# Optimization experiments

Hardware: AMD Instinct MI355X
Metric: run time of the kernel (lower is better)

Reference implementation:

```python
import jax, jax.numpy as jnp
import numpy as np

DIM = 1024
NUM_HEADS = 8
HEAD_DIM = 64
QK_DIM = NUM_HEADS * HEAD_DIM  # 512
B, S = 4, 1024


def setup_inputs() -> dict:
    key = jax.random.key(0)
    k1, k2, k3, k4, k5 = jax.random.split(key, 5)
    x = jax.random.normal(k1, (B, S, DIM), dtype=jnp.float32)
    mask = jax.random.randint(k2, (B, S), 0, 2).astype(bool)
    rotator = jax.random.normal(k3, (B, S, HEAD_DIM, HEAD_DIM), dtype=jnp.float32)
    # Linear weights stored as [in, out] for x @ W
    w_t = jax.random.normal(k4, (DIM, 2 * QK_DIM + DIM), dtype=jnp.float32) * (DIM ** -0.5)
    w_o = jax.random.normal(k5, (DIM, DIM), dtype=jnp.float32) * (DIM ** -0.5)
    return {"x": x, "mask": mask, "rotator": rotator, "w_t": w_t, "w_o": w_o}


def taylor_atn_fn(qs, ks, vs, mask):
    # 2nd-order Taylor approximation of softmax attention:
    # exp(s) ~= 1 + s + s^2/2, with invalid keys masked out.
    scale = HEAD_DIM ** -0.5
    s = jnp.einsum('bqhd,bkhd->bhqk', qs, ks) * scale  # [B,H,S,S]
    scores = 1.0 + s + 0.5 * s * s
    scores = scores * mask[:, None, None, :].astype(scores.dtype)  # mask keys
    denom = jnp.maximum(jnp.sum(scores, axis=-1), 1e-6)            # [B,H,Q]
    out = jnp.einsum('bhqk,bkhd->bqhd', scores, vs)
    out = out / jnp.transpose(denom, (0, 2, 1))[..., None]         # [B,Q,H,vd]
    return out.reshape(out.shape[0], out.shape[1], -1)


def reference(x, mask, rotator, w_t, w_o):
    t = x @ w_t                                   # [B,S,2*QK+DIM]
    Bx, Sx = t.shape[0], t.shape[1]
    qs = t[..., :QK_DIM].reshape(Bx, Sx, NUM_HEADS, HEAD_DIM)
    ks = t[..., QK_DIM:2 * QK_DIM].reshape(Bx, Sx, NUM_HEADS, HEAD_DIM)
    vs = t[..., 2 * QK_DIM:].reshape(Bx, Sx, NUM_HEADS, -1)
    m = mask[..., None, None]
    # masked per-position rotation: q -> R q, k -> R^T k
    qs = jnp.where(m, jnp.einsum('bsij,bshj->bshi', rotator, qs), qs)
    ks = jnp.where(m, jnp.einsum('bsij,bshi->bshj', rotator, ks), ks)
    out = taylor_atn_fn(qs, ks, vs, mask)
    return out @ w_o
```

## Files before the change

### kernel.cpp

```cpp
#include <hip/hip_runtime.h>
#include <cstdint>
#include <cstddef>

#define DIMX  1024
#define NH    8
#define HD    64
#define QKD   512
#define VDD   128
#define BATCH 4
#define SEQ   1024
#define NPOS  (BATCH*SEQ)
#define TW    (2*QKD + DIMX)
#define SCALE 0.125f

typedef __bf16 bf16x8 __attribute__((ext_vector_type(8)));
typedef float  f32x4  __attribute__((ext_vector_type(4)));
typedef float  f32x16 __attribute__((ext_vector_type(16)));

__device__ __forceinline__ ushort f2bf(float f) {
    unsigned b = __float_as_uint(f);
    return (ushort)((b + 0x7FFFu + ((b >> 16) & 1u)) >> 16);
}
__device__ __forceinline__ float bf2f(ushort u) {
    return __uint_as_float((unsigned)u << 16);
}

__device__ __forceinline__ unsigned cvtpk(float lo, float hi) {
    unsigned r;
    asm("v_cvt_pk_bf16_f32 %0, %1, %2" : "=v"(r) : "v"(lo), "v"(hi));
    return r;
}

__device__ __forceinline__ void plswap(unsigned &a, unsigned &b) {
    asm("v_permlane32_swap_b32 %0, %1" : "+v"(a), "+v"(b));
}

#define GLD16(src, dst) __builtin_amdgcn_global_load_lds(                      \
    (const __attribute__((address_space(1))) unsigned int*)(src),              \
    (__attribute__((address_space(3))) unsigned int*)(dst), 16, 0, 0)

#define SW(row, col) ((row)*64 + ((col) ^ (((row)&7)<<3)))

__device__ __forceinline__ int2 xcd_swz(int gx, int gy) {
    const int nwg = gx * gy;
    int id = blockIdx.y * gx + blockIdx.x;
    id = (id & 7) * (nwg >> 3) + (id >> 3);
    return make_int2(id % gx, id / gx);
}

__global__ __launch_bounds__(256)
void cast_bf16(const float* __restrict__ in, ushort* __restrict__ out, int n4)
{
    const int i = blockIdx.x * 256 + threadIdx.x;
    if (i >= n4) return;
    float4 v = *(const float4*)(in + (size_t)i * 4);
    ushort4 o;
    o.x = f2bf(v.x); o.y = f2bf(v.y); o.z = f2bf(v.z); o.w = f2bf(v.w);
    *(ushort4*)(out + (size_t)i * 4) = o;
}

__global__ __launch_bounds__(256)
void transpose_cast(const float* __restrict__ W, ushort* __restrict__ WT,
                    int K, int N)
{
    __shared__ float tile[32][33];
    const int bn = blockIdx.x * 32;
    const int bk = blockIdx.y * 32;
    const int tx = threadIdx.x & 31;
    const int ty = threadIdx.x >> 5;
    #pragma unroll
    for (int i = ty; i < 32; i += 8)
        tile[i][tx] = W[(size_t)(bk + i) * N + bn + tx];
    __syncthreads();
    #pragma unroll
    for (int i = ty; i < 32; i += 8)
        WT[(size_t)(bn + i) * K + bk + tx] = f2bf(tile[tx][i]);
}

__global__ __launch_bounds__(256, 2)
void gemm_qkv(const ushort* __restrict__ A, const ushort* __restrict__ BT,
              ushort* __restrict__ t1b, ushort* __restrict__ Vt)
{
    const int K = DIMX, N = TW;
    __shared__ __align__(16) ushort lA[128 * 32];
    __shared__ __align__(16) ushort lB[128 * 32];

    const int2 bij = xcd_swz(N/128, NPOS/128);
    const int tid  = threadIdx.x;
    const int lane = tid & 63;
    const int wave = tid >> 6;
    const int wr   = wave >> 1;
    const int wc   = wave & 1;
    const int bm   = bij.y * 128;
    const int bn   = bij.x * 128;

    const int r0 = wave * 32 + (lane >> 2);
    const int kc = (lane & 3) * 8;
    const ushort* a0 = A  + (size_t)(bm + r0) * K + kc;
    const ushort* a1 = A  + (size_t)(bm + r0 + 16) * K + kc;
    const ushort* b0 = BT + (size_t)(bn + r0) * K + kc;
    const ushort* b1 = BT + (size_t)(bn + r0 + 16) * K + kc;
    ushort* lA0 = lA + wave * 1024;
    ushort* lA1 = lA0 + 512;
    ushort* lB0 = lB + wave * 1024;
    ushort* lB1 = lB0 + 512;

    const int fr = lane & 15;
    const int kh = (lane >> 4) * 8;
    const ushort* ra = lA + (wr * 64 + fr) * 32 + kh;
    const ushort* rb = lB + (wc * 64 + fr) * 32 + kh;

    f32x4 acc[4][4] = {};

    for (int k0 = 0; k0 < K; k0 += 32) {
        GLD16(a0 + k0, lA0);
        GLD16(a1 + k0, lA1);
        GLD16(b0 + k0, lB0);
        GLD16(b1 + k0, lB1);
        asm volatile("s_waitcnt vmcnt(0)" ::: "memory");
        __syncthreads();
        bf16x8 af[4], bfr[4];
        #pragma unroll
        for (int m = 0; m < 4; ++m) af[m]  = *(const bf16x8*)(ra + m * 512);
        #pragma unroll
        for (int n = 0; n < 4; ++n) bfr[n] = *(const bf16x8*)(rb + n * 512);
        #pragma unroll
        for (int m = 0; m < 4; ++m)
            #pragma unroll
            for (int n = 0; n < 4; ++n)
                acc[m][n] = __builtin_amdgcn_mfma_f32_16x16x32_bf16(
                    af[m], bfr[n], acc[m][n], 0, 0, 0);
        __syncthreads();
    }

    const int orow = (lane >> 4) * 4;
    if (bn < 1024) {
        #pragma unroll
        for (int m = 0; m < 4; ++m)
            #pragma unroll
            for (int n = 0; n < 4; ++n) {
                ushort* dst = t1b + (size_t)(bm + wr * 64 + m * 16 + orow) * 1024
                                  + bn + wc * 64 + n * 16 + fr;
                #pragma unroll
                for (int q = 0; q < 4; ++q)
                    dst[(size_t)q * 1024] = f2bf(acc[m][n][q]);
            }
    } else {
        #pragma unroll
        for (int m = 0; m < 4; ++m)
            #pragma unroll
            for (int n = 0; n < 4; ++n) {
                const int row0 = bm + wr * 64 + m * 16 + orow;
                const int cv   = bn + wc * 64 + n * 16 + fr - 1024;
                const int hh = cv >> 7, vd = cv & 127;
                const int bb = row0 >> 10, ss = row0 & 1023;
                ushort o4[4];
                #pragma unroll
                for (int q = 0; q < 4; ++q) o4[q] = f2bf(acc[m][n][q]);
                *(ushort4*)&Vt[((size_t)(bb*NH + hh)*VDD + vd)*SEQ + ss] =
                    *(ushort4*)o4;
            }
    }
}

__global__ __launch_bounds__(256, 2)
void gemm_bf16_mfma(const ushort* __restrict__ A, const ushort* __restrict__ BT,
                    float* __restrict__ C, int M, int N, int K)
{
    __shared__ __align__(16) ushort lA[128 * 32];
    __shared__ __align__(16) ushort lB[128 * 32];

    const int2 bij = xcd_swz(N/128, M/128);
    const int tid  = threadIdx.x;
    const int lane = tid & 63;
    const int wave = tid >> 6;
    const int wr   = wave >> 1;
    const int wc   = wave & 1;
    const int bm   = bij.y * 128;
    const int bn   = bij.x * 128;

    const int r0 = wave * 32 + (lane >> 2);
    const int kc = (lane & 3) * 8;
    const ushort* a0 = A  + (size_t)(bm + r0) * K + kc;
    const ushort* a1 = A  + (size_t)(bm + r0 + 16) * K + kc;
    const ushort* b0 = BT + (size_t)(bn + r0) * K + kc;
    const ushort* b1 = BT + (size_t)(bn + r0 + 16) * K + kc;
    ushort* lA0 = lA + wave * 1024;
    ushort* lA1 = lA0 + 512;
    ushort* lB0 = lB + wave * 1024;
    ushort* lB1 = lB0 + 512;

    const int fr = lane & 15;
    const int kh = (lane >> 4) * 8;
    const ushort* ra = lA + (wr * 64 + fr) * 32 + kh;
    const ushort* rb = lB + (wc * 64 + fr) * 32 + kh;

    f32x4 acc[4][4] = {};

    for (int k0 = 0; k0 < K; k0 += 32) {
        GLD16(a0 + k0, lA0);
        GLD16(a1 + k0, lA1);
        GLD16(b0 + k0, lB0);
        GLD16(b1 + k0, lB1);
        asm volatile("s_waitcnt vmcnt(0)" ::: "memory");
        __syncthreads();
        bf16x8 af[4], bfr[4];
        #pragma unroll
        for (int m = 0; m < 4; ++m) af[m]  = *(const bf16x8*)(ra + m * 512);
        #pragma unroll
        for (int n = 0; n < 4; ++n) bfr[n] = *(const bf16x8*)(rb + n * 512);
        #pragma unroll
        for (int m = 0; m < 4; ++m)
            #pragma unroll
            for (int n = 0; n < 4; ++n)
                acc[m][n] = __builtin_amdgcn_mfma_f32_16x16x32_bf16(
                    af[m], bfr[n], acc[m][n], 0, 0, 0);
        __syncthreads();
    }

    const int orow = (lane >> 4) * 4;
    #pragma unroll
    for (int m = 0; m < 4; ++m)
        #pragma unroll
        for (int n = 0; n < 4; ++n) {
            float* dst = C + (size_t)(bm + wr * 64 + m * 16 + orow) * N
                           + bn + wc * 64 + n * 16 + fr;
            #pragma unroll
            for (int q = 0; q < 4; ++q)
                dst[(size_t)q * N] = acc[m][n][q];
        }
}

__global__ __launch_bounds__(256)
void rotate_pack_qk(const ushort* __restrict__ t1b, const int* __restrict__ mask,
                    const float* __restrict__ rot, ushort* __restrict__ Qb,
                    ushort* __restrict__ Kb)
{
    const int p   = blockIdx.x;
    const int tid = threadIdx.x;
    const int b = p >> 10, s = p & 1023;
    const bool rotated = (mask[p] != 0);

    __shared__ float R[64][69];
    __shared__ float qv[QKD];
    __shared__ float kv[QKD];

    const ushort* tq = t1b + (size_t)p * 1024;
    {
        ushort2 q2 = *(const ushort2*)(tq + tid*2);
        ushort2 k2 = *(const ushort2*)(tq + QKD + tid*2);
        qv[tid*2]   = bf2f(q2.x); qv[tid*2+1] = bf2f(q2.y);
        kv[tid*2]   = bf2f(k2.x); kv[tid*2+1] = bf2f(k2.y);
        if (rotated) {
            const float* Rg = rot + (size_t)p * 4096;
            const int base = tid * 16;
            const int r = base >> 6, c = base & 63;
            #pragma unroll
            for (int x = 0; x < 16; x += 4) {
                float4 v = *(const float4*)(Rg + base + x);
                R[r][c+x+0] = v.x; R[r][c+x+1] = v.y;
                R[r][c+x+2] = v.z; R[r][c+x+3] = v.w;
            }
        }
    }
    __syncthreads();

    #pragma unroll
    for (int ph = 0; ph < 2; ++ph) {
        const int h = (tid >> 6) + ph*4;
        const int i = tid & 63;
        const float* qh  = &qv[h*64];
        const float* kh2 = &kv[h*64];
        float aq, ak;
        if (rotated) {
            aq = 0.f; ak = 0.f;
            #pragma unroll 8
            for (int j = 0; j < 64; ++j) {
                aq = fmaf(R[i][j], qh[j], aq);
                ak = fmaf(R[j][i], kh2[j], ak);
            }
        } else {
            aq = qh[i]; ak = kh2[i];
        }
        const size_t dst = ((size_t)(b*NH + h)*SEQ + s)*HD + i;
        Qb[dst] = f2bf(aq * SCALE);
        Kb[dst] = f2bf(ak);
    }
}

__global__ __launch_bounds__(256, 2)
void taylor_attn_mfma(const ushort* __restrict__ Qb, const ushort* __restrict__ Kb,
                      const ushort* __restrict__ Vt, const int* __restrict__ mask,
                      ushort* __restrict__ attn)
{
    const int bh  = blockIdx.x;
    const int qt  = blockIdx.y;
    const int b   = bh >> 3, h = bh & 7;
    const int tid = threadIdx.x;
    const int lane = tid & 63;
    const int wave = tid >> 6;
    const int kh  = wave >> 1;
    const int qg  = wave & 1;
    const int l31 = lane & 31;
    const int g   = lane >> 5;

    __shared__ __align__(16) ushort smem[32768];
    __shared__ float mskAll[SEQ];
    __shared__ float dpart[64];
    __shared__ float dinv2[64];

    ushort* Ksp = smem + kh * 8192;
    ushort* Vsp = smem + 16384 + kh * 8192;
    float*  comb = (float*)smem;

    {
        int4 mv = *(const int4*)(mask + b*SEQ + tid*4);
        float4 f = make_float4(mv.x ? 1.f : 0.f, mv.y ? 1.f : 0.f,
                               mv.z ? 1.f : 0.f, mv.w ? 1.f : 0.f);
        *(float4*)&mskAll[tid*4] = f;
    }

    const ushort* qrow = Qb + ((size_t)bh*SEQ + qt*64 + qg*32 + l31) * HD + g*8;
    bf16x8 qf[4];
    #pragma unroll
    for (int ds = 0; ds < 4; ++ds) qf[ds] = *(const bf16x8*)(qrow + ds*16);

    const int sub  = lane >> 3;
    const int scol = ((lane & 7) * 8) ^ (sub << 3);
    const ushort* Kbase = Kb + (size_t)bh*SEQ*HD;
    const ushort* Vbase = Vt + (size_t)bh*VDD*SEQ;

#define ISSUE_K(buf, ktn) do {                                                 \
    _Pragma("unroll")                                                          \
    for (int i_ = 0; i_ < 4; ++i_)                                             \
        GLD16(Kbase + ((size_t)(ktn)*64 + 8*(qg*4+i_) + sub)*HD + scol,        \
              Ksp + (buf)*4096 + (qg*4+i_)*512);                               \
} while (0)
#define ISSUE_V(ktn) do {                                                      \
    _Pragma("unroll")                                                          \
    for (int i_ = 0; i_ < 8; ++i_)                                             \
        GLD16(Vbase + (size_t)(8*(qg*8+i_) + sub)*SEQ + (ktn)*64 + scol,       \
              Vsp + (qg*8+i_)*512);                                            \
} while (0)

    f32x16 acc[4] = {};
    float dacc = 0.f;

    __syncthreads();
    ISSUE_K(0, kh*8);

    for (int it = 0; it < 8; ++it) {
        const int kt = kh*8 + it;
        const int cb = it & 1;
        ISSUE_V(kt);
        if (it < 7) {
            ISSUE_K(cb ^ 1, kt + 1);
            asm volatile("s_waitcnt vmcnt(12)" ::: "memory");
        } else {
            asm volatile("s_waitcnt vmcnt(8)"  ::: "memory");
        }
        __builtin_amdgcn_s_barrier();

        f32x16 sf0 = {}, sf1 = {};
        __builtin_amdgcn_s_setprio(1);
        #pragma unroll
        for (int ds = 0; ds < 4; ++ds) {
            const int dc = ds*16 + g*8;
            bf16x8 kf0 = *(const bf16x8*)&Ksp[cb*4096 + SW(l31, dc)];
            bf16x8 kf1 = *(const bf16x8*)&Ksp[cb*4096 + SW(32 + l31, dc)];
            sf0 = __builtin_amdgcn_mfma_f32_32x32x16_bf16(kf0, qf[ds], sf0, 0, 0, 0);
            sf1 = __builtin_amdgcn_mfma_f32_32x32x16_bf16(kf1, qf[ds], sf1, 0, 0, 0);
        }
        __builtin_amdgcn_s_setprio(0);

        const float* mrow = mskAll + kt*64;
        unsigned w0[8], w1[8];
        float dadd = 0.f;
        #pragma unroll
        for (int rr = 0; rr < 4; ++rr) {
            const float4 mqa = *(const float4*)&mrow[8*rr + 4*g];
            const float4 mqb = *(const float4*)&mrow[32 + 8*rr + 4*g];
            float s0 = sf0[rr*4+0], s1 = sf0[rr*4+1];
            float s2 = sf0[rr*4+2], s3 = sf0[rr*4+3];
            float c0 = fmaf(fmaf(0.5f*s0, s0, s0), mqa.x, mqa.x);
            float c1 = fmaf(fmaf(0.5f*s1, s1, s1), mqa.y, mqa.y);
            float c2 = fmaf(fmaf(0.5f*s2, s2, s2), mqa.z, mqa.z);
            float c3 = fmaf(fmaf(0.5f*s3, s3, s3), mqa.w, mqa.w);
            float t0 = sf1[rr*4+0], t1 = sf1[rr*4+1];
            float t2 = sf1[rr*4+2], t3 = sf1[rr*4+3];
            float d0 = fmaf(fmaf(0.5f*t0, t0, t0), mqb.x, mqb.x);
            float d1 = fmaf(fmaf(0.5f*t1, t1, t1), mqb.y, mqb.y);
            float d2 = fmaf(fmaf(0.5f*t2, t2, t2), mqb.z, mqb.z);
            float d3 = fmaf(fmaf(0.5f*t3, t3, t3), mqb.w, mqb.w);
            dadd += ((c0+c1)+(c2+c3)) + ((d0+d1)+(d2+d3));
            w0[rr*2+0] = cvtpk(c0, c1);
            w0[rr*2+1] = cvtpk(c2, c3);
            w1[rr*2+0] = cvtpk(d0, d1);
            w1[rr*2+1] = cvtpk(d2, d3);
        }
        dacc += dadd;
        plswap(w0[0], w0[2]); plswap(w0[1], w0[3]);
        plswap(w0[4], w0[6]); plswap(w0[5], w0[7]);
        plswap(w1[0], w1[2]); plswap(w1[1], w1[3]);
        plswap(w1[4], w1[6]); plswap(w1[5], w1[7]);

        if (it < 7) asm volatile("s_waitcnt vmcnt(4)" ::: "memory");
        else        asm volatile("s_waitcnt vmcnt(0)" ::: "memory");
        __builtin_amdgcn_s_barrier();

        __builtin_amdgcn_s_setprio(1);
        #pragma unroll
        for (int kq = 0; kq < 4; ++kq) {
            union { unsigned u[4]; bf16x8 v; } pu;
            if (kq == 0)      { pu.u[0]=w0[0]; pu.u[1]=w0[1]; pu.u[2]=w0[2]; pu.u[3]=w0[3]; }
            else if (kq == 1) { pu.u[0]=w0[4]; pu.u[1]=w0[5]; pu.u[2]=w0[6]; pu.u[3]=w0[7]; }
            else if (kq == 2) { pu.u[0]=w1[0]; pu.u[1]=w1[1]; pu.u[2]=w1[2]; pu.u[3]=w1[3]; }
            else              { pu.u[0]=w1[4]; pu.u[1]=w1[5]; pu.u[2]=w1[6]; pu.u[3]=w1[7]; }
            const int kcol = kq*16 + g*8;
            acc[0] = __builtin_amdgcn_mfma_f32_32x32x16_bf16(
                pu.v, *(const bf16x8*)&Vsp[SW(      l31, kcol)], acc[0], 0, 0, 0);
            acc[1] = __builtin_amdgcn_mfma_f32_32x32x16_bf16(
                pu.v, *(const bf16x8*)&Vsp[SW( 32 + l31, kcol)], acc[1], 0, 0, 0);
            acc[2] = __builtin_amdgcn_mfma_f32_32x32x16_bf16(
                pu.v, *(const bf16x8*)&Vsp[SW( 64 + l31, kcol)], acc[2], 0, 0, 0);
            acc[3] = __builtin_amdgcn_mfma_f32_32x32x16_bf16(
                pu.v, *(const bf16x8*)&Vsp[SW( 96 + l31, kcol)], acc[3], 0, 0, 0);
        }
        __builtin_amdgcn_s_setprio(0);
        __builtin_amdgcn_s_barrier();
    }
#undef ISSUE_K
#undef ISSUE_V

    const float dhalf = dacc + __shfl_xor(dacc, 32);

    if (kh == 1) {
        float* cbp = comb + qg * 4096;
        #pragma unroll
        for (int vb = 0; vb < 4; ++vb)
            #pragma unroll
            for (int rr = 0; rr < 4; ++rr) {
                float4 v = make_float4(acc[vb][rr*4+0], acc[vb][rr*4+1],
                                       acc[vb][rr*4+2], acc[vb][rr*4+3]);
                *(float4*)&cbp[(vb*32 + l31)*32 + 4*g + 8*rr] = v;
            }
        if (lane < 32) dpart[qg*32 + l31] = dhalf;
    }
    __syncthreads();
    if (kh == 0) {
        float* cbp = comb + qg * 4096;
        const float dtot = dhalf + dpart[qg*32 + l31];
        if (lane < 32) dinv2[qg*32 + l31] = 1.f / fmaxf(dtot, 1e-6f);
        #pragma unroll
        for (int vb = 0; vb < 4; ++vb)
            #pragma unroll
            for (int rr = 0; rr < 4; ++rr) {
                float4 v = *(const float4*)&cbp[(vb*32 + l31)*32 + 4*g + 8*rr];
                acc[vb][rr*4+0] += v.x; acc[vb][rr*4+1] += v.y;
                acc[vb][rr*4+2] += v.z; acc[vb][rr*4+3] += v.w;
            }
        float inv[16];
        #pragma unroll
        for (int rr = 0; rr < 4; ++rr) {
            float4 iv = *(const float4*)&dinv2[qg*32 + 8*rr + 4*g];
            inv[rr*4+0] = iv.x; inv[rr*4+1] = iv.y;
            inv[rr*4+2] = iv.z; inv[rr*4+3] = iv.w;
        }
        ushort* obase = attn + ((size_t)(b*SEQ + qt*64 + qg*32)) * DIMX
                      + h*VDD + l31;
        #pragma unroll
        for (int vb = 0; vb < 4; ++vb)
            #pragma unroll
            for (int rr = 0; rr < 4; ++rr)
                #pragma unroll
                for (int j = 0; j < 4; ++j) {
                    const int q = 4*g + 8*rr + j;
                    obase[(size_t)q*DIMX + vb*32] = f2bf(acc[vb][rr*4+j] * inv[rr*4+j]);
                }
    }
}

extern "C" void kernel_launch(void* const* d_in, const int* in_sizes, int n_in,
                              void* d_out, int out_size, void* d_ws, size_t ws_size,
                              hipStream_t stream)
{
    const float* x    = (const float*)d_in[0];
    const int*   mask = (const int*)d_in[1];
    const float* rot  = (const float*)d_in[2];
    const float* w_t  = (const float*)d_in[3];
    const float* w_o  = (const float*)d_in[4];
    float* out = (float*)d_out;

    ushort* t1b    = (ushort*)d_ws;
    ushort* xbf    = t1b + (size_t)NPOS * 1024;
    ushort* attnbf = xbf;
    ushort* wtT    = xbf + (size_t)NPOS * DIMX;
    ushort* woT    = wtT + (size_t)TW * DIMX;
    ushort* Qb     = woT + (size_t)DIMX * DIMX;
    ushort* Kb     = Qb  + (size_t)BATCH * NH * SEQ * HD;
    ushort* Vtp    = Kb  + (size_t)BATCH * NH * SEQ * HD;

    cast_bf16<<<(NPOS*DIMX/4 + 255)/256, 256, 0, stream>>>(x, xbf, NPOS*DIMX/4);
    transpose_cast<<<dim3(TW/32, DIMX/32),   256, 0, stream>>>(w_t, wtT, DIMX, TW);
    transpose_cast<<<dim3(DIMX/32, DIMX/32), 256, 0, stream>>>(w_o, woT, DIMX, DIMX);

    gemm_qkv<<<dim3(TW/128, NPOS/128), 256, 0, stream>>>(xbf, wtT, t1b, Vtp);
    rotate_pack_qk<<<NPOS, 256, 0, stream>>>(t1b, mask, rot, Qb, Kb);
    taylor_attn_mfma<<<dim3(BATCH*NH, SEQ/64), 256, 0, stream>>>(Qb, Kb, Vtp, mask, attnbf);
    gemm_bf16_mfma<<<dim3(DIMX/128, NPOS/128), 256, 0, stream>>>(attnbf, woT, out, NPOS, DIMX, DIMX);
}
```

Measured before the change: 111.4 us.

## Restructure Taylor attention to 2 waves each owning full key range

The attention kernel drops from 4 waves (split across two key halves plus two query groups) to 2 waves, each handling 32 queries over all 1024 keys in 32-key tiles with its own private K/V LDS buffers. This removes the cross-wave block barriers inside the loop and the final LDS reduction of partial accumulators and denominators. V tiles use a new 32-column swizzle. In exchange, each workgroup has half as many waves, the per-wave loop is longer, and the serialized waitcnt pattern per iteration may expose more memory latency.

After: 120.6 us. 1.08x slower.

```diff
diff --git a/kernel.cpp b/kernel.cpp
--- a/kernel.cpp
+++ b/kernel.cpp
@@ -40,6 +40,7 @@
     (__attribute__((address_space(3))) unsigned int*)(dst), 16, 0, 0)
 
 #define SW(row, col) ((row)*64 + ((col) ^ (((row)&7)<<3)))
+#define SW32(row, col) ((row)*32 + ((col) ^ ((((row)>>1)&3)<<3)))
 
 __device__ __forceinline__ int2 xcd_swz(int gx, int gy) {
     const int nwg = gx * gy;
@@ -288,7 +289,7 @@
     }
 }
 
-__global__ __launch_bounds__(256, 2)
+__global__ __launch_bounds__(128, 2)
 void taylor_attn_mfma(const ushort* __restrict__ Qb, const ushort* __restrict__ Kb,
                       const ushort* __restrict__ Vt, const int* __restrict__ mask,
                       ushort* __restrict__ attn)
@@ -299,185 +300,141 @@
     const int tid = threadIdx.x;
     const int lane = tid & 63;
     const int wave = tid >> 6;
-    const int kh  = wave >> 1;
-    const int qg  = wave & 1;
     const int l31 = lane & 31;
     const int g   = lane >> 5;
 
-    __shared__ __align__(16) ushort smem[32768];
+    __shared__ __align__(16) ushort smem[16384];
     __shared__ float mskAll[SEQ];
-    __shared__ float dpart[64];
-    __shared__ float dinv2[64];
-
-    ushort* Ksp = smem + kh * 8192;
-    ushort* Vsp = smem + 16384 + kh * 8192;
-    float*  comb = (float*)smem;
+    __shared__ float dinvw[2][32];
+
+    ushort* Ksp = smem + wave * 4096;
+    ushort* Vsp = smem + 8192 + wave * 4096;
 
     {
-        int4 mv = *(const int4*)(mask + b*SEQ + tid*4);
-        float4 f = make_float4(mv.x ? 1.f : 0.f, mv.y ? 1.f : 0.f,
-                               mv.z ? 1.f : 0.f, mv.w ? 1.f : 0.f);
-        *(float4*)&mskAll[tid*4] = f;
-    }
-
-    const ushort* qrow = Qb + ((size_t)bh*SEQ + qt*64 + qg*32 + l31) * HD + g*8;
+        int4 m0 = *(const int4*)(mask + b*SEQ + tid*8);
+        int4 m1 = *(const int4*)(mask + b*SEQ + tid*8 + 4);
+        float4 f0 = make_float4(m0.x ? 1.f : 0.f, m0.y ? 1.f : 0.f,
+                                m0.z ? 1.f : 0.f, m0.w ? 1.f : 0.f);
+        float4 f1 = make_float4(m1.x ? 1.f : 0.f, m1.y ? 1.f : 0.f,
+                                m1.z ? 1.f : 0.f, m1.w ? 1.f : 0.f);
+        *(float4*)&mskAll[tid*8]     = f0;
+        *(float4*)&mskAll[tid*8 + 4] = f1;
+    }
+
+    const ushort* qrow = Qb + ((size_t)bh*SEQ + qt*64 + wave*32 + l31) * HD + g*8;
     bf16x8 qf[4];
     #pragma unroll
     for (int ds = 0; ds < 4; ++ds) qf[ds] = *(const bf16x8*)(qrow + ds*16);
 
-    const int sub  = lane >> 3;
-    const int scol = ((lane & 7) * 8) ^ (sub << 3);
+    const int ksub  = lane >> 3;
+    const int kcolS = ((lane & 7) * 8) ^ (ksub << 3);
+    const int vrow  = lane >> 2;
+    const int vcolS = ((lane & 3) * 8) ^ (((lane >> 3) & 3) << 3);
     const ushort* Kbase = Kb + (size_t)bh*SEQ*HD;
     const ushort* Vbase = Vt + (size_t)bh*VDD*SEQ;
 
 #define ISSUE_K(buf, ktn) do {                                                 \
     _Pragma("unroll")                                                          \
     for (int i_ = 0; i_ < 4; ++i_)                                             \
-        GLD16(Kbase + ((size_t)(ktn)*64 + 8*(qg*4+i_) + sub)*HD + scol,        \
-              Ksp + (buf)*4096 + (qg*4+i_)*512);                               \
+        GLD16(Kbase + ((size_t)(ktn)*32 + 8*i_ + ksub)*HD + kcolS,             \
+              Ksp + (buf)*2048 + i_*512);                                      \
 } while (0)
 #define ISSUE_V(ktn) do {                                                      \
     _Pragma("unroll")                                                          \
     for (int i_ = 0; i_ < 8; ++i_)                                             \
-        GLD16(Vbase + (size_t)(8*(qg*8+i_) + sub)*SEQ + (ktn)*64 + scol,       \
-              Vsp + (qg*8+i_)*512);                                            \
+        GLD16(Vbase + (size_t)(16*i_ + vrow)*SEQ + (ktn)*32 + vcolS,           \
+              Vsp + i_*512);                                                   \
 } while (0)
 
     f32x16 acc[4] = {};
     float dacc = 0.f;
 
     __syncthreads();
-    ISSUE_K(0, kh*8);
-
-    for (int it = 0; it < 8; ++it) {
-        const int kt = kh*8 + it;
-        const int cb = it & 1;
+    ISSUE_K(0, 0);
+    asm volatile("s_waitcnt vmcnt(0)" ::: "memory");
+
+    #pragma unroll 2
+    for (int kt = 0; kt < 32; ++kt) {
+        const int cb = kt & 1;
+        asm volatile("s_waitcnt lgkmcnt(0)" ::: "memory");
         ISSUE_V(kt);
-        if (it < 7) {
-            ISSUE_K(cb ^ 1, kt + 1);
-            asm volatile("s_waitcnt vmcnt(12)" ::: "memory");
-        } else {
-            asm volatile("s_waitcnt vmcnt(8)"  ::: "memory");
-        }
-        __builtin_amdgcn_s_barrier();
-
-        f32x16 sf0 = {}, sf1 = {};
+        if (kt < 31) ISSUE_K(cb ^ 1, kt + 1);
+
+        f32x16 sf0 = {};
         __builtin_amdgcn_s_setprio(1);
         #pragma unroll
         for (int ds = 0; ds < 4; ++ds) {
-            const int dc = ds*16 + g*8;
-            bf16x8 kf0 = *(const bf16x8*)&Ksp[cb*4096 + SW(l31, dc)];
-            bf16x8 kf1 = *(const bf16x8*)&Ksp[cb*4096 + SW(32 + l31, dc)];
-            sf0 = __builtin_amdgcn_mfma_f32_32x32x16_bf16(kf0, qf[ds], sf0, 0, 0, 0);
-            sf1 = __builtin_amdgcn_mfma_f32_32x32x16_bf16(kf1, qf[ds], sf1, 0, 0, 0);
+            bf16x8 kf = *(const bf16x8*)&Ksp[cb*2048 + SW(l31, ds*16 + g*8)];
+            sf0 = __builtin_amdgcn_mfma_f32_32x32x16_bf16(kf, qf[ds], sf0, 0, 0, 0);
         }
         __builtin_amdgcn_s_setprio(0);
 
-        const float* mrow = mskAll + kt*64;
-        unsigned w0[8], w1[8];
+        const float* mrow = mskAll + kt*32;
+        unsigned w[8];
         float dadd = 0.f;
         #pragma unroll
         for (int rr = 0; rr < 4; ++rr) {
-            const float4 mqa = *(const float4*)&mrow[8*rr + 4*g];
-            const float4 mqb = *(const float4*)&mrow[32 + 8*rr + 4*g];
+            const float4 mq = *(const float4*)&mrow[8*rr + 4*g];
             float s0 = sf0[rr*4+0], s1 = sf0[rr*4+1];
             float s2 = sf0[rr*4+2], s3 = sf0[rr*4+3];
-            float c0 = fmaf(fmaf(0.5f*s0, s0, s0), mqa.x, mqa.x);
-            float c1 = fmaf(fmaf(0.5f*s1, s1, s1), mqa.y, mqa.y);
-            float c2 = fmaf(fmaf(0.5f*s2, s2, s2), mqa.z, mqa.z);
-            float c3 = fmaf(fmaf(0.5f*s3, s3, s3), mqa.w, mqa.w);
-            float t0 = sf1[rr*4+0], t1 = sf1[rr*4+1];
-            float t2 = sf1[rr*4+2], t3 = sf1[rr*4+3];
-            float d0 = fmaf(fmaf(0.5f*t0, t0, t0), mqb.x, mqb.x);
-            float d1 = fmaf(fmaf(0.5f*t1, t1, t1), mqb.y, mqb.y);
-            float d2 = fmaf(fmaf(0.5f*t2, t2, t2), mqb.z, mqb.z);
-            float d3 = fmaf(fmaf(0.5f*t3, t3, t3), mqb.w, mqb.w);
-            dadd += ((c0+c1)+(c2+c3)) + ((d0+d1)+(d2+d3));
-            w0[rr*2+0] = cvtpk(c0, c1);
-            w0[rr*2+1] = cvtpk(c2, c3);
-            w1[rr*2+0] = cvtpk(d0, d1);
-            w1[rr*2+1] = cvtpk(d2, d3);
+            float c0 = fmaf(fmaf(0.5f*s0, s0, s0), mq.x, mq.x);
+            float c1 = fmaf(fmaf(0.5f*s1, s1, s1), mq.y, mq.y);
+            float c2 = fmaf(fmaf(0.5f*s2, s2, s2), mq.z, mq.z);
+            float c3 = fmaf(fmaf(0.5f*s3, s3, s3), mq.w, mq.w);
+            dadd += (c0 + c1) + (c2 + c3);
+            w[rr*2+0] = cvtpk(c0, c1);
+            w[rr*2+1] = cvtpk(c2, c3);
         }
         dacc += dadd;
-        plswap(w0[0], w0[2]); plswap(w0[1], w0[3]);
-        plswap(w0[4], w0[6]); plswap(w0[5], w0[7]);
-        plswap(w1[0], w1[2]); plswap(w1[1], w1[3]);
-        plswap(w1[4], w1[6]); plswap(w1[5], w1[7]);
-
-        if (it < 7) asm volatile("s_waitcnt vmcnt(4)" ::: "memory");
-        else        asm volatile("s_waitcnt vmcnt(0)" ::: "memory");
-        __builtin_amdgcn_s_barrier();
+        plswap(w[0], w[2]); plswap(w[1], w[3]);
+        plswap(w[4], w[6]); plswap(w[5], w[7]);
+
+        if (kt < 31) asm volatile("s_waitcnt vmcnt(4)" ::: "memory");
+        else         asm volatile("s_waitcnt vmcnt(0)" ::: "memory");
 
         __builtin_amdgcn_s_setprio(1);
         #pragma unroll
-        for (int kq = 0; kq < 4; ++kq) {
+        for (int kq = 0; kq < 2; ++kq) {
             union { unsigned u[4]; bf16x8 v; } pu;
-            if (kq == 0)      { pu.u[0]=w0[0]; pu.u[1]=w0[1]; pu.u[2]=w0[2]; pu.u[3]=w0[3]; }
-            else if (kq == 1) { pu.u[0]=w0[4]; pu.u[1]=w0[5]; pu.u[2]=w0[6]; pu.u[3]=w0[7]; }
-            else if (kq == 2) { pu.u[0]=w1[0]; pu.u[1]=w1[1]; pu.u[2]=w1[2]; pu.u[3]=w1[3]; }
-            else              { pu.u[0]=w1[4]; pu.u[1]=w1[5]; pu.u[2]=w1[6]; pu.u[3]=w1[7]; }
+            if (kq == 0) { pu.u[0]=w[0]; pu.u[1]=w[1]; pu.u[2]=w[2]; pu.u[3]=w[3]; }
+            else         { pu.u[0]=w[4]; pu.u[1]=w[5]; pu.u[2]=w[6]; pu.u[3]=w[7]; }
             const int kcol = kq*16 + g*8;
             acc[0] = __builtin_amdgcn_mfma_f32_32x32x16_bf16(
-                pu.v, *(const bf16x8*)&Vsp[SW(      l31, kcol)], acc[0], 0, 0, 0);
+                pu.v, *(const bf16x8*)&Vsp[SW32(      l31, kcol)], acc[0], 0, 0, 0);
             acc[1] = __builtin_amdgcn_mfma_f32_32x32x16_bf16(
-                pu.v, *(const bf16x8*)&Vsp[SW( 32 + l31, kcol)], acc[1], 0, 0, 0);
+                pu.v, *(const bf16x8*)&Vsp[SW32( 32 + l31, kcol)], acc[1], 0, 0, 0);
             acc[2] = __builtin_amdgcn_mfma_f32_32x32x16_bf16(
-                pu.v, *(const bf16x8*)&Vsp[SW( 64 + l31, kcol)], acc[2], 0, 0, 0);
+                pu.v, *(const bf16x8*)&Vsp[SW32( 64 + l31, kcol)], acc[2], 0, 0, 0);
             acc[3] = __builtin_amdgcn_mfma_f32_32x32x16_bf16(
-                pu.v, *(const bf16x8*)&Vsp[SW( 96 + l31, kcol)], acc[3], 0, 0, 0);
+                pu.v, *(const bf16x8*)&Vsp[SW32( 96 + l31, kcol)], acc[3], 0, 0, 0);
         }
         __builtin_amdgcn_s_setprio(0);
-        __builtin_amdgcn_s_barrier();
+        if (kt < 31) asm volatile("s_waitcnt vmcnt(0)" ::: "memory");
     }
 #undef ISSUE_K
 #undef ISSUE_V
 
-    const float dhalf = dacc + __shfl_xor(dacc, 32);
-
-    if (kh == 1) {
-        float* cbp = comb + qg * 4096;
-        #pragma unroll
-        for (int vb = 0; vb < 4; ++vb)
-            #pragma unroll
-            for (int rr = 0; rr < 4; ++rr) {
-                float4 v = make_float4(acc[vb][rr*4+0], acc[vb][rr*4+1],
-                                       acc[vb][rr*4+2], acc[vb][rr*4+3]);
-                *(float4*)&cbp[(vb*32 + l31)*32 + 4*g + 8*rr] = v;
+    const float dfull = dacc + __shfl_xor(dacc, 32);
+    if (lane < 32) dinvw[wave][l31] = 1.f / fmaxf(dfull, 1e-6f);
+    float inv[16];
+    #pragma unroll
+    for (int rr = 0; rr < 4; ++rr) {
+        float4 iv = *(const float4*)&dinvw[wave][8*rr + 4*g];
+        inv[rr*4+0] = iv.x; inv[rr*4+1] = iv.y;
+        inv[rr*4+2] = iv.z; inv[rr*4+3] = iv.w;
+    }
+
+    ushort* obase = attn + ((size_t)(b*SEQ + qt*64 + wave*32)) * DIMX
+                  + h*VDD + l31;
+    #pragma unroll
+    for (int vb = 0; vb < 4; ++vb)
+        #pragma unroll
+        for (int rr = 0; rr < 4; ++rr)
+            #pragma unroll
+            for (int j = 0; j < 4; ++j) {
+                const int q = 4*g + 8*rr + j;
+                obase[(size_t)q*DIMX + vb*32] = f2bf(acc[vb][rr*4+j] * inv[rr*4+j]);
             }
-        if (lane < 32) dpart[qg*32 + l31] = dhalf;
-    }
-    __syncthreads();
-    if (kh == 0) {
-        float* cbp = comb + qg * 4096;
-        const float dtot = dhalf + dpart[qg*32 + l31];
-        if (lane < 32) dinv2[qg*32 + l31] = 1.f / fmaxf(dtot, 1e-6f);
-        #pragma unroll
-        for (int vb = 0; vb < 4; ++vb)
-            #pragma unroll
-            for (int rr = 0; rr < 4; ++rr) {
-                float4 v = *(const float4*)&cbp[(vb*32 + l31)*32 + 4*g + 8*rr];
-                acc[vb][rr*4+0] += v.x; acc[vb][rr*4+1] += v.y;
-                acc[vb][rr*4+2] += v.z; acc[vb][rr*4+3] += v.w;
-            }
-        float inv[16];
-        #pragma unroll
-        for (int rr = 0; rr < 4; ++rr) {
-            float4 iv = *(const float4*)&dinv2[qg*32 + 8*rr + 4*g];
-            inv[rr*4+0] = iv.x; inv[rr*4+1] = iv.y;
-            inv[rr*4+2] = iv.z; inv[rr*4+3] = iv.w;
-        }
-        ushort* obase = attn + ((size_t)(b*SEQ + qt*64 + qg*32)) * DIMX
-                      + h*VDD + l31;
-        #pragma unroll
-        for (int vb = 0; vb < 4; ++vb)
-            #pragma unroll
-            for (int rr = 0; rr < 4; ++rr)
-                #pragma unroll
-                for (int j = 0; j < 4; ++j) {
-                    const int q = 4*g + 8*rr + j;
-                    obase[(size_t)q*DIMX + vb*32] = f2bf(acc[vb][rr*4+j] * inv[rr*4+j]);
-                }
-    }
 }
 
 extern "C" void kernel_launch(void* const* d_in, const int* in_sizes, int n_in,
@@ -506,6 +463,6 @@
 
     gemm_qkv<<<dim3(TW/128, NPOS/128), 256, 0, stream>>>(xbf, wtT, t1b, Vtp);
     rotate_pack_qk<<<NPOS, 256, 0, stream>>>(t1b, mask, rot, Qb, Kb);
-    taylor_attn_mfma<<<dim3(BATCH*NH, SEQ/64), 256, 0, stream>>>(Qb, Kb, Vtp, mask, attnbf);
+    taylor_attn_mfma<<<dim3(BATCH*NH, SEQ/64), 128, 0, stream>>>(Qb, Kb, Vtp, mask, attnbf);
     gemm_bf16_mfma<<<dim3(DIMX/128, NPOS/128), 256, 0, stream>>>(attnbf, woT, out, NPOS, DIMX, DIMX);
 }
```

## Merge prep kernels and widen GEMM K-tile to 64 with swizzled LDS

Applied to the files above, without the earlier changes.

Replaces the three preprocessing launches (x cast and two weight transposes) with one prep_all kernel that dispatches on block index, which removes two launches. Both GEMMs now stage 64-wide K tiles with XOR-swizzled LDS addressing instead of 32-wide. This halves the barrier and wait iterations and is meant to reduce LDS bank conflicts on fragment reads. Shared memory per block doubles to 32KB, which could limit occupancy.

Result: faster. 98.34 us (-11.7%).

```diff
diff --git a/kernel.cpp b/kernel.cpp
--- a/kernel.cpp
+++ b/kernel.cpp
@@ -49,23 +49,31 @@
 }
 
 __global__ __launch_bounds__(256)
-void cast_bf16(const float* __restrict__ in, ushort* __restrict__ out, int n4)
-{
-    const int i = blockIdx.x * 256 + threadIdx.x;
-    if (i >= n4) return;
-    float4 v = *(const float4*)(in + (size_t)i * 4);
-    ushort4 o;
-    o.x = f2bf(v.x); o.y = f2bf(v.y); o.z = f2bf(v.z); o.w = f2bf(v.w);
-    *(ushort4*)(out + (size_t)i * 4) = o;
-}
-
-__global__ __launch_bounds__(256)
-void transpose_cast(const float* __restrict__ W, ushort* __restrict__ WT,
-                    int K, int N)
+void prep_all(const float* __restrict__ x, const float* __restrict__ w_t,
+              const float* __restrict__ w_o, ushort* __restrict__ xbf,
+              ushort* __restrict__ wtT, ushort* __restrict__ woT)
 {
     __shared__ float tile[32][33];
-    const int bn = blockIdx.x * 32;
-    const int bk = blockIdx.y * 32;
+    const int bid = blockIdx.x;
+    if (bid < 2048) {
+        const size_t i = ((size_t)bid * 256 + threadIdx.x) * 8;
+        float4 v0 = *(const float4*)(x + i);
+        float4 v1 = *(const float4*)(x + i + 4);
+        ushort o[8] = {f2bf(v0.x), f2bf(v0.y), f2bf(v0.z), f2bf(v0.w),
+                       f2bf(v1.x), f2bf(v1.y), f2bf(v1.z), f2bf(v1.w)};
+        *(uint4*)(xbf + i) = *(uint4*)o;
+        return;
+    }
+    const float* W; ushort* WT; int K, N, bn, bk;
+    if (bid < 4096) {
+        W = w_t; WT = wtT; K = DIMX; N = TW;
+        const int t = bid - 2048;
+        bn = (t & 63) * 32; bk = (t >> 6) * 32;
+    } else {
+        W = w_o; WT = woT; K = DIMX; N = DIMX;
+        const int t = bid - 4096;
+        bn = (t & 31) * 32; bk = (t >> 5) * 32;
+    }
     const int tx = threadIdx.x & 31;
     const int ty = threadIdx.x >> 5;
     #pragma unroll
@@ -77,63 +85,65 @@
         WT[(size_t)(bn + i) * K + bk + tx] = f2bf(tile[tx][i]);
 }
 
+#define GEMM_PROLOGUE(Aptr, Bptr, Kdim)                                        \
+    __shared__ __align__(16) ushort lA[128 * 64];                              \
+    __shared__ __align__(16) ushort lB[128 * 64];                              \
+    const int tid  = threadIdx.x;                                              \
+    const int lane = tid & 63;                                                 \
+    const int wave = tid >> 6;                                                 \
+    const int wr   = wave >> 1;                                                \
+    const int wc   = wave & 1;                                                 \
+    const int rsub = lane >> 3;                        \
+    const int scol = ((lane & 7) * 8) ^ ((rsub & 7) << 3);                     \
+    const ushort* aP = (Aptr) + (size_t)(bm + wave*32 + rsub) * (Kdim) + scol; \
+    const ushort* bP = (Bptr) + (size_t)(bn + wave*32 + rsub) * (Kdim) + scol; \
+    ushort* lAw = lA + wave * 2048;                                            \
+    ushort* lBw = lB + wave * 2048;                                            \
+    const int fr = lane & 15;                                                  \
+    const int l4 = lane >> 4;                                                  \
+    f32x4 acc[4][4] = {};
+
+#define GEMM_KLOOP(Kdim)                                                       \
+    for (int k0 = 0; k0 < (Kdim); k0 += 64) {                                  \
+        _Pragma("unroll")                                                      \
+        for (int c = 0; c < 4; ++c) {                                          \
+            GLD16(aP + (size_t)(c*8) * (Kdim) + k0, lAw + c*512);              \
+            GLD16(bP + (size_t)(c*8) * (Kdim) + k0, lBw + c*512);              \
+        }                                                                      \
+        asm volatile("s_waitcnt vmcnt(0)" ::: "memory");                       \
+        __syncthreads();                                                       \
+        _Pragma("unroll")                                                      \
+        for (int ks = 0; ks < 2; ++ks) {                                       \
+            bf16x8 af[4], bfr[4];                                              \
+            _Pragma("unroll")                                                  \
+            for (int m = 0; m < 4; ++m)                                        \
+                af[m] = *(const bf16x8*)&lA[SW(wr*64 + m*16 + fr,              \
+                                               ks*32 + l4*8)];                 \
+            _Pragma("unroll")                                                  \
+            for (int n = 0; n < 4; ++n)                                        \
+                bfr[n] = *(const bf16x8*)&lB[SW(wc*64 + n*16 + fr,             \
+                                                ks*32 + l4*8)];               \
+            _Pragma("unroll")                                                  \
+            for (int m = 0; m < 4; ++m)                                        \
+                _Pragma("unroll")                                              \
+                for (int n = 0; n < 4; ++n)                                    \
+                    acc[m][n] = __builtin_amdgcn_mfma_f32_16x16x32_bf16(       \
+                        af[m], bfr[n], acc[m][n], 0, 0, 0);                    \
+        }                                                                      \
+        __syncthreads();                                                       \
+    }
+
 __global__ __launch_bounds__(256, 2)
 void gemm_qkv(const ushort* __restrict__ A, const ushort* __restrict__ BT,
               ushort* __restrict__ t1b, ushort* __restrict__ Vt)
 {
-    const int K = DIMX, N = TW;
-    __shared__ __align__(16) ushort lA[128 * 32];
-    __shared__ __align__(16) ushort lB[128 * 32];
-
-    const int2 bij = xcd_swz(N/128, NPOS/128);
-    const int tid  = threadIdx.x;
-    const int lane = tid & 63;
-    const int wave = tid >> 6;
-    const int wr   = wave >> 1;
-    const int wc   = wave & 1;
-    const int bm   = bij.y * 128;
-    const int bn   = bij.x * 128;
-
-    const int r0 = wave * 32 + (lane >> 2);
-    const int kc = (lane & 3) * 8;
-    const ushort* a0 = A  + (size_t)(bm + r0) * K + kc;
-    const ushort* a1 = A  + (size_t)(bm + r0 + 16) * K + kc;
-    const ushort* b0 = BT + (size_t)(bn + r0) * K + kc;
-    const ushort* b1 = BT + (size_t)(bn + r0 + 16) * K + kc;
-    ushort* lA0 = lA + wave * 1024;
-    ushort* lA1 = lA0 + 512;
-    ushort* lB0 = lB + wave * 1024;
-    ushort* lB1 = lB0 + 512;
-
-    const int fr = lane & 15;
-    const int kh = (lane >> 4) * 8;
-    const ushort* ra = lA + (wr * 64 + fr) * 32 + kh;
-    const ushort* rb = lB + (wc * 64 + fr) * 32 + kh;
-
-    f32x4 acc[4][4] = {};
-
-    for (int k0 = 0; k0 < K; k0 += 32) {
-        GLD16(a0 + k0, lA0);
-        GLD16(a1 + k0, lA1);
-        GLD16(b0 + k0, lB0);
-        GLD16(b1 + k0, lB1);
-        asm volatile("s_waitcnt vmcnt(0)" ::: "memory");
-        __syncthreads();
-        bf16x8 af[4], bfr[4];
-        #pragma unroll
-        for (int m = 0; m < 4; ++m) af[m]  = *(const bf16x8*)(ra + m * 512);
-        #pragma unroll
-        for (int n = 0; n < 4; ++n) bfr[n] = *(const bf16x8*)(rb + n * 512);
-        #pragma unroll
-        for (int m = 0; m < 4; ++m)
-            #pragma unroll
-            for (int n = 0; n < 4; ++n)
-                acc[m][n] = __builtin_amdgcn_mfma_f32_16x16x32_bf16(
-                    af[m], bfr[n], acc[m][n], 0, 0, 0);
-        __syncthreads();
-    }
-
-    const int orow = (lane >> 4) * 4;
+    const int2 bij = xcd_swz(TW/128, NPOS/128);
+    const int bm = bij.y * 128;
+    const int bn = bij.x * 128;
+    GEMM_PROLOGUE(A, BT, DIMX)
+    GEMM_KLOOP(DIMX)
+
+    const int orow = l4 * 4;
     if (bn < 1024) {
         #pragma unroll
         for (int m = 0; m < 4; ++m)
@@ -165,69 +175,24 @@
 
 __global__ __launch_bounds__(256, 2)
 void gemm_bf16_mfma(const ushort* __restrict__ A, const ushort* __restrict__ BT,
-                    float* __restrict__ C, int M, int N, int K)
-{
-    __shared__ __align__(16) ushort lA[128 * 32];
-    __shared__ __align__(16) ushort lB[128 * 32];
-
-    const int2 bij = xcd_swz(N/128, M/128);
-    const int tid  = threadIdx.x;
-    const int lane = tid & 63;
-    const int wave = tid >> 6;
-    const int wr   = wave >> 1;
-    const int wc   = wave & 1;
-    const int bm   = bij.y * 128;
-    const int bn   = bij.x * 128;
-
-    const int r0 = wave * 32 + (lane >> 2);
-    const int kc = (lane & 3) * 8;
-    const ushort* a0 = A  + (size_t)(bm + r0) * K + kc;
-    const ushort* a1 = A  + (size_t)(bm + r0 + 16) * K + kc;
-    const ushort* b0 = BT + (size_t)(bn + r0) * K + kc;
-    const ushort* b1 = BT + (size_t)(bn + r0 + 16) * K + kc;
-    ushort* lA0 = lA + wave * 1024;
-    ushort* lA1 = lA0 + 512;
-    ushort* lB0 = lB + wave * 1024;
-    ushort* lB1 = lB0 + 512;
-
-    const int fr = lane & 15;
-    const int kh = (lane >> 4) * 8;
-    const ushort* ra = lA + (wr * 64 + fr) * 32 + kh;
-    const ushort* rb = lB + (wc * 64 + fr) * 32 + kh;
-
-    f32x4 acc[4][4] = {};
-
-    for (int k0 = 0; k0 < K; k0 += 32) {
-        GLD16(a0 + k0, lA0);
-        GLD16(a1 + k0, lA1);
-        GLD16(b0 + k0, lB0);
-        GLD16(b1 + k0, lB1);
-        asm volatile("s_waitcnt vmcnt(0)" ::: "memory");
-        __syncthreads();
-        bf16x8 af[4], bfr[4];
-        #pragma unroll
-        for (int m = 0; m < 4; ++m) af[m]  = *(const bf16x8*)(ra + m * 512);
-        #pragma unroll
-        for (int n = 0; n < 4; ++n) bfr[n] = *(const bf16x8*)(rb + n * 512);
-        #pragma unroll
-        for (int m = 0; m < 4; ++m)
-            #pragma unroll
-            for (int n = 0; n < 4; ++n)
-                acc[m][n] = __builtin_amdgcn_mfma_f32_16x16x32_bf16(
-                    af[m], bfr[n], acc[m][n], 0, 0, 0);
-        __syncthreads();
-    }
-
-    const int orow = (lane >> 4) * 4;
+                    float* __restrict__ C)
+{
+    const int2 bij = xcd_swz(DIMX/128, NPOS/128);
+    const int bm = bij.y * 128;
+    const int bn = bij.x * 128;
+    GEMM_PROLOGUE(A, BT, DIMX)
+    GEMM_KLOOP(DIMX)
+
+    const int orow = l4 * 4;
     #pragma unroll
     for (int m = 0; m < 4; ++m)
         #pragma unroll
         for (int n = 0; n < 4; ++n) {
-            float* dst = C + (size_t)(bm + wr * 64 + m * 16 + orow) * N
+            float* dst = C + (size_t)(bm + wr * 64 + m * 16 + orow) * DIMX
                            + bn + wc * 64 + n * 16 + fr;
             #pragma unroll
             for (int q = 0; q < 4; ++q)
-                dst[(size_t)q * N] = acc[m][n][q];
+                dst[(size_t)q * DIMX] = acc[m][n][q];
         }
 }
 
@@ -500,12 +465,10 @@
     ushort* Kb     = Qb  + (size_t)BATCH * NH * SEQ * HD;
     ushort* Vtp    = Kb  + (size_t)BATCH * NH * SEQ * HD;
 
-    cast_bf16<<<(NPOS*DIMX/4 + 255)/256, 256, 0, stream>>>(x, xbf, NPOS*DIMX/4);
-    transpose_cast<<<dim3(TW/32, DIMX/32),   256, 0, stream>>>(w_t, wtT, DIMX, TW);
-    transpose_cast<<<dim3(DIMX/32, DIMX/32), 256, 0, stream>>>(w_o, woT, DIMX, DIMX);
+    prep_all<<<5120, 256, 0, stream>>>(x, w_t, w_o, xbf, wtT, woT);
 
     gemm_qkv<<<dim3(TW/128, NPOS/128), 256, 0, stream>>>(xbf, wtT, t1b, Vtp);
     rotate_pack_qk<<<NPOS, 256, 0, stream>>>(t1b, mask, rot, Qb, Kb);
     taylor_attn_mfma<<<dim3(BATCH*NH, SEQ/64), 256, 0, stream>>>(Qb, Kb, Vtp, mask, attnbf);
-    gemm_bf16_mfma<<<dim3(DIMX/128, NPOS/128), 256, 0, stream>>>(attnbf, woT, out, NPOS, DIMX, DIMX);
-}
+    gemm_bf16_mfma<<<dim3(DIMX/128, NPOS/128), 256, 0, stream>>>(attnbf, woT, out);
+}
```
